# Optimization experiments

Hardware: AMD Instinct MI355X
Metric: run time of the kernel (lower is better)

Reference implementation:

```python
import jax, jax.numpy as jnp
import numpy as np

B, N, M, C, H = 2, 256, 512, 256, 8
Dh = C // H          # head dim = 32
F = 256              # frequency_embedding_size
MAX_PERIOD = 10000.0


def setup_inputs() -> dict:
    rng = jax.random.key(0)
    ks = jax.random.split(rng, 12)
    s = 0.02

    def w(k, shape):
        return jax.random.normal(k, shape, jnp.float32) * s

    inp = {
        "query": jax.random.normal(ks[0], (B, N, C), jnp.float32),
        "key": jax.random.normal(ks[1], (B, M, C), jnp.float32),
        "query_pos": jax.random.uniform(ks[2], (B, N, M), jnp.float32),
        # attention projections (torch Linear stores W as (out,in))
        "Wq": w(ks[3], (C, C)), "bq": jnp.zeros((C,), jnp.float32),
        "Wk": w(ks[4], (C, C)),
        "Wv": w(ks[5], (C, C)), "bv": jnp.zeros((C,), jnp.float32),
        "Wo": w(ks[6], (C, C)), "bo": jnp.zeros((C,), jnp.float32),
        # ScalarEmbedder MLP: Linear(F, C) -> SiLU -> Linear(C, C)
        "W1": w(ks[7], (C, F)), "b1": jnp.zeros((C,), jnp.float32),
        "W2": w(ks[8], (C, C)), "b2": jnp.zeros((C,), jnp.float32),
        "freqs": jnp.exp(-np.log(MAX_PERIOD) * jnp.arange(F // 2, dtype=jnp.float32) / (F // 2)),
    }
    return inp


def reference(query, key, query_pos, Wq, bq, Wk, Wv, bv, Wo, bo, W1, b1, W2, b2, freqs):
    scale = Dh ** (-0.5)
    # projections -> (B, H, N/M, Dh)
    q = (query @ Wq.T + bq).reshape(B, N, H, Dh).transpose(0, 2, 1, 3)
    k = (key @ Wk.T).reshape(B, M, H, Dh).transpose(0, 2, 1, 3)
    v = (key @ Wv.T + bv).reshape(B, M, H, Dh).transpose(0, 2, 1, 3)
    # scalar positional embedding per (n, m) pair
    t = query_pos.reshape(-1)                              # (B*N*M,)
    tf = t[:, None] * freqs                                # (B*N*M, F/2)
    emb = jnp.concatenate([jnp.cos(tf), jnp.sin(tf)], -1)  # (B*N*M, F)
    pe = jax.nn.silu(emb @ W1.T + b1) @ W2.T + b2          # (B*N*M, C)
    pe = pe.reshape(B, N, M, H, Dh).transpose(0, 3, 1, 2, 4)  # (B,H,N,M,Dh)
    # gated scores: (q[:,:,:,None] * pe) . k  ==  einsum over d
    attn = jnp.einsum('bhnd,bhnmd,bhmd->bhnm', q, pe, k) * scale
    attn = jax.nn.softmax(attn, axis=-1)
    x = jnp.einsum('bhnm,bhmd->bhnd', attn, v)             # (B,H,N,Dh)
    x = x.transpose(0, 2, 1, 3).reshape(B, N, C)
    return x @ Wo.T + bo + query
```

## Files before the change

kernel.cpp:

```cpp
#include <hip/hip_runtime.h>

#define Bn 2
#define Nn 256
#define Mn 512
#define Cn 256
#define Hn 8
#define MT 64
#define SCALE_ 0.17677669529663687f
#define INV2PI 0.15915494309189535f

typedef short bf16x8 __attribute__((ext_vector_type(8)));
typedef short bf16x4 __attribute__((ext_vector_type(4)));
typedef float f32x4 __attribute__((ext_vector_type(4)));

static __device__ __forceinline__ float b2f(short s) {
    unsigned u = ((unsigned)(unsigned short)s) << 16;
    return __builtin_bit_cast(float, u);
}
static __device__ __forceinline__ short f2b(float f) {
    unsigned u = __builtin_bit_cast(unsigned, f);
    u += 0x7fffu + ((u >> 16) & 1u);
    return (short)(u >> 16);
}
static __device__ __forceinline__ void async16(const void* g, void* l) {
    __builtin_amdgcn_global_load_lds(
        (const __attribute__((address_space(1))) unsigned int*)g,
        (__attribute__((address_space(3))) unsigned int*)l, 16, 0, 0);
}

__global__ __launch_bounds__(256) void prep(
        const float* __restrict__ query, const float* __restrict__ key,
        const float* __restrict__ Wq, const float* __restrict__ bq,
        const float* __restrict__ Wk, const float* __restrict__ Wv,
        const float* __restrict__ bv, const float* __restrict__ W1,
        const float* __restrict__ W2, short* __restrict__ W1b,
        short* __restrict__ W2b, float* __restrict__ qp,
        short* __restrict__ kpb, short* __restrict__ vpb) {
    __shared__ float arow[32][Cn];
    const int bid = blockIdx.x;
    const int t = threadIdx.x;
    if (bid < 256) {
        const int i = bid * 256 + t;
        W1b[i] = f2b(W1[i]);
        W2b[i] = f2b(W2[i]);
        return;
    }
    if (bid < 512) {
        const int id = bid - 256;
        const int r0 = (id >> 2) * 8, c0 = (id & 3) * 64;
        #pragma unroll
        for (int i = 0; i < 8; ++i) arow[i][t] = query[(size_t)(r0 + i) * Cn + t];
        __syncthreads();
        const int col = c0 + (t & 63);
        const int rs = t >> 6;
        float a0 = 0.f, a1 = 0.f;
        const float* wr = Wq + (size_t)col * Cn;
        for (int k = 0; k < Cn; k += 4) {
            const float4 wv = *(const float4*)(wr + k);
            const int r = rs * 2;
            a0 += arow[r][k] * wv.x + arow[r][k+1] * wv.y
                + arow[r][k+2] * wv.z + arow[r][k+3] * wv.w;
            a1 += arow[r+1][k] * wv.x + arow[r+1][k+1] * wv.y
                + arow[r+1][k+2] * wv.z + arow[r+1][k+3] * wv.w;
        }
        const float bvv = bq[col];
        qp[(size_t)(r0 + rs * 2) * Cn + col] = a0 + bvv;
        qp[(size_t)(r0 + rs * 2 + 1) * Cn + col] = a1 + bvv;
        return;
    }
    const int isv = bid >= 768;
    const int id = bid - (isv ? 768 : 512);
    const int r0 = (id >> 3) * 32, c0 = (id & 7) * 32;
    const float* W = isv ? Wv : Wk;
    short* outb = isv ? vpb : kpb;
    #pragma unroll
    for (int i = 0; i < 32; ++i) arow[i][t] = key[(size_t)(r0 + i) * Cn + t];
    __syncthreads();
    const int col = c0 + (t & 31);
    const int rs = t >> 5;
    float a4[4] = {0.f, 0.f, 0.f, 0.f};
    const float* wr = W + (size_t)col * Cn;
    for (int k = 0; k < Cn; k += 4) {
        const float4 wv = *(const float4*)(wr + k);
        #pragma unroll
        for (int i = 0; i < 4; ++i) {
            const int r = rs * 4 + i;
            a4[i] += arow[r][k] * wv.x + arow[r][k+1] * wv.y
                   + arow[r][k+2] * wv.z + arow[r][k+3] * wv.w;
        }
    }
    const float bvv = isv ? bv[col] : 0.f;
    const int bk = r0 >> 9, m0 = (r0 & 511) + rs * 4;
    char* base = (char*)outb + (size_t)bk * Mn * Cn * 2;
    #pragma unroll
    for (int i = 0; i < 4; ++i) {
        const int m = m0 + i;
        *(short*)(base + m * 512 + ((col * 2) ^ ((m & 7) << 4))) = f2b(a4[i] + bvv);
    }
}

__global__ __launch_bounds__(512)
__attribute__((amdgpu_waves_per_eu(2, 2)))
void fused_attn(
        const float* __restrict__ qp, const short* __restrict__ kpb,
        const short* __restrict__ vpb, const float* __restrict__ qpos,
        const short* __restrict__ W1b, const short* __restrict__ W2b,
        const float* __restrict__ b1, const float* __restrict__ b2,
        const float* __restrict__ freqs, const float* __restrict__ Wo,
        const float* __restrict__ bo, const float* __restrict__ query,
        float* __restrict__ xout) {
    __shared__ __align__(16) char embS[MT * 512];
    __shared__ __align__(16) char kS[MT * 512];
    __shared__ __align__(16) char vS[MT * 512];
    __shared__ float tposS[Mn];
    __shared__ float fbuf[128];
    __shared__ float scb2[Hn * MT];
    __shared__ float pacc[512];
    __shared__ float corrS[Hn], lS[Hn];

    const int t = threadIdx.x;
    const int lane = t & 63;
    const int w = t >> 6;
    const int lr = lane & 15, lg = lane >> 4;

    const int qrow = ((blockIdx.x & 7) << 6) | (blockIdx.x >> 3);
    const int b = qrow >> 8;

    const int cA = w * 32 + lr, cB = cA + 16;
    const short* w1p0 = W1b + (size_t)cA * Cn + lg * 8;
    const short* w1p1 = W1b + (size_t)cB * Cn + lg * 8;
    const short* w2p0 = W2b + (size_t)cA * Cn + lg * 8;
    const short* w2p1 = W2b + (size_t)cB * Cn + lg * 8;

    bf16x8 wreg[16];
    #pragma unroll
    for (int kk = 0; kk < 8; ++kk) {
        wreg[kk] = *(const bf16x8*)(w1p0 + kk * 32);
        wreg[8 + kk] = *(const bf16x8*)(w1p1 + kk * 32);
    }

    const float b1v0 = b1[cA], b1v1 = b1[cB];
    float qr[8], b2r[8];
    #pragma unroll
    for (int i = 0; i < 8; ++i) {
        const int c = w * 32 + (i >> 2) * 16 + lg * 4 + (i & 3);
        qr[i] = qp[(size_t)qrow * Cn + c] * SCALE_;
        b2r[i] = b2[c];
    }
    tposS[t] = qpos[(size_t)qrow * Mn + t];
    if (t < 128) fbuf[t] = freqs[t] * INV2PI;
    float m_run = -1e30f, l_run = 0.f;
    float xacc = 0.f;
    __syncthreads();

    for (int m0 = 0; m0 < Mn; m0 += MT) {
        {
            const size_t tbase = ((size_t)(b * Mn + m0)) * Cn * 2;
            #pragma unroll
            for (int i = 0; i < 4; ++i) {
                const int seg = (i * 8 + w) * 1024;
                async16((const char*)kpb + tbase + seg + lane * 16, kS + seg);
                async16((const char*)vpb + tbase + seg + lane * 16, vS + seg);
            }
        }

        {
            const int m = t >> 3, fg = t & 7;
            const float tv = tposS[m0 + m];
            bf16x8 pc[2], ps[2];
            #pragma unroll
            for (int j = 0; j < 16; ++j) {
                const float xr = tv * fbuf[fg * 16 + j];
                pc[j >> 3][j & 7] = f2b(__builtin_amdgcn_cosf(xr));
                ps[j >> 3][j & 7] = f2b(__builtin_amdgcn_sinf(xr));
            }
            char* rowp = embS + m * 512;
            const int sw = (m & 7) << 4;
            *(bf16x8*)(rowp + ((fg * 32) ^ sw)) = pc[0];
            *(bf16x8*)(rowp + ((fg * 32 + 16) ^ sw)) = pc[1];
            *(bf16x8*)(rowp + ((256 + fg * 32) ^ sw)) = ps[0];
            *(bf16x8*)(rowp + ((256 + fg * 32 + 16) ^ sw)) = ps[1];
        }
        __syncthreads();

        f32x4 acc[4][2];
        #pragma unroll
        for (int pb = 0; pb < 4; ++pb) {
            acc[pb][0] = (f32x4){0.f, 0.f, 0.f, 0.f};
            acc[pb][1] = (f32x4){0.f, 0.f, 0.f, 0.f};
        }
        #pragma unroll
        for (int pb = 0; pb < 4; ++pb) {
            const int row = pb * 16 + lr;
            const int sw = (row & 7) << 4;
            const char* rowp = embS + row * 512;
            #pragma unroll
            for (int kk = 0; kk < 8; ++kk) {
                const bf16x8 a = *(const bf16x8*)(rowp + ((lg * 16 + kk * 64) ^ sw));
                acc[pb][0] = __builtin_amdgcn_mfma_f32_16x16x32_bf16(a, wreg[kk],     acc[pb][0], 0, 0, 0);
                acc[pb][1] = __builtin_amdgcn_mfma_f32_16x16x32_bf16(a, wreg[8 + kk], acc[pb][1], 0, 0, 0);
            }
        }
        #pragma unroll
        for (int kk = 0; kk < 8; ++kk) {
            wreg[kk] = *(const bf16x8*)(w2p0 + kk * 32);
            wreg[8 + kk] = *(const bf16x8*)(w2p1 + kk * 32);
        }
        __syncthreads();

        #pragma unroll
        for (int pb = 0; pb < 4; ++pb) {
            #pragma unroll
            for (int jb = 0; jb < 2; ++jb) {
                const float bv = jb ? b1v1 : b1v0;
                const int j = w * 32 + jb * 16 + lr;
                #pragma unroll
                for (int r = 0; r < 4; ++r) {
                    const int row = pb * 16 + lg * 4 + r;
                    float hv = acc[pb][jb][r] + bv;
                    hv = hv / (1.f + __expf(-hv));
                    *(short*)(embS + row * 512 + ((j * 2) ^ ((row & 7) << 4))) = f2b(hv);
                }
            }
        }
        __syncthreads();

        #pragma unroll
        for (int mb = 0; mb < 4; ++mb)
            #pragma unroll
            for (int cb = 0; cb < 2; ++cb)
                #pragma unroll
                for (int r = 0; r < 4; ++r)
                    acc[mb][cb][r] = b2r[cb * 4 + r];
        #pragma unroll
        for (int mb = 0; mb < 4; ++mb) {
            const int row = mb * 16 + lr;
            const int sw = (row & 7) << 4;
            const char* rowp = embS + row * 512;
            #pragma unroll
            for (int kk = 0; kk < 8; ++kk) {
                const bf16x8 a = *(const bf16x8*)(rowp + ((lg * 16 + kk * 64) ^ sw));
                acc[mb][0] = __builtin_amdgcn_mfma_f32_16x16x32_bf16(wreg[kk],     a, acc[mb][0], 0, 0, 0);
                acc[mb][1] = __builtin_amdgcn_mfma_f32_16x16x32_bf16(wreg[8 + kk], a, acc[mb][1], 0, 0, 0);
            }
        }
        #pragma unroll
        for (int kk = 0; kk < 8; ++kk) {
            wreg[kk] = *(const bf16x8*)(w1p0 + kk * 32);
            wreg[8 + kk] = *(const bf16x8*)(w1p1 + kk * 32);
        }

        #pragma unroll
        for (int mb = 0; mb < 4; ++mb) {
            const int m = mb * 16 + lr;
            const int sw = (m & 7) << 4;
            const char* kr = kS + m * 512;
            const int c0 = (w * 32 + lg * 4) * 2;
            const bf16x4 k0 = *(const bf16x4*)(kr + (c0 ^ sw));
            const bf16x4 k1 = *(const bf16x4*)(kr + ((c0 + 32) ^ sw));
            float partial = 0.f;
            #pragma unroll
            for (int r = 0; r < 4; ++r) {
                partial += qr[r] * b2f(k0[r]) * acc[mb][0][r]
                         + qr[4 + r] * b2f(k1[r]) * acc[mb][1][r];
            }
            partial += __shfl_xor(partial, 16);
            partial += __shfl_xor(partial, 32);
            if (lg == 0) scb2[w * MT + m] = partial;
        }

        {
            const float s = scb2[w * MT + lane];
            float tmax = s;
            #pragma unroll
            for (int msk = 1; msk < 64; msk <<= 1) tmax = fmaxf(tmax, __shfl_xor(tmax, msk));
            const float mnew = fmaxf(m_run, tmax);
            const float corr = __expf(m_run - mnew);
            const float e = __expf(s - mnew);
            scb2[w * MT + lane] = e;
            float ss = e;
            #pragma unroll
            for (int msk = 1; msk < 64; msk <<= 1) ss += __shfl_xor(ss, msk);
            l_run = l_run * corr + ss;
            m_run = mnew;
            if (lane == 0) corrS[w] = corr;
        }
        __syncthreads();

        {
            const int c = t & 255, half = t >> 8;
            const int h = c >> 5;
            const int cx = c * 2;
            const char* vb = vS + (half * 32) * 512;
            const float* wr2 = scb2 + h * MT + half * 32;
            float s = 0.f;
            #pragma unroll
            for (int i = 0; i < 8; ++i) {
                const float4 wa = *(const float4*)(wr2 + i * 4);
                const int mb4 = i * 4;
                s += wa.x * b2f(*(const short*)(vb + (mb4 + 0) * 512 + (cx ^ (((mb4 + 0) & 7) << 4))))
                   + wa.y * b2f(*(const short*)(vb + (mb4 + 1) * 512 + (cx ^ (((mb4 + 1) & 7) << 4))))
                   + wa.z * b2f(*(const short*)(vb + (mb4 + 2) * 512 + (cx ^ (((mb4 + 2) & 7) << 4))))
                   + wa.w * b2f(*(const short*)(vb + (mb4 + 3) * 512 + (cx ^ (((mb4 + 3) & 7) << 4))));
            }
            pacc[t] = s;
        }
        __syncthreads();
        if (t < 256) xacc = xacc * corrS[t >> 5] + pacc[t] + pacc[t + 256];
    }

    if (lane == 0) lS[w] = l_run;
    __syncthreads();
    if (t < 256) scb2[t] = xacc / lS[t >> 5];
    __syncthreads();
    {
        const int j = t & 255, half = t >> 8;
        const float* wr = Wo + (size_t)j * Cn + half * 128;
        const float* xb = scb2 + half * 128;
        float s = 0.f;
        for (int k = 0; k < 128; k += 4) {
            const float4 wv = *(const float4*)(wr + k);
            s += xb[k] * wv.x + xb[k+1] * wv.y + xb[k+2] * wv.z + xb[k+3] * wv.w;
        }
        pacc[t] = s;
    }
    __syncthreads();
    if (t < 256)
        xout[(size_t)qrow * Cn + t] = pacc[t] + pacc[t + 256] + bo[t]
                                    + query[(size_t)qrow * Cn + t];
}

extern "C" void kernel_launch(void* const* d_in, const int* in_sizes, int n_in,
                              void* d_out, int out_size, void* d_ws, size_t ws_size,
                              hipStream_t stream) {
    const float* query = (const float*)d_in[0];
    const float* key   = (const float*)d_in[1];
    const float* qpos  = (const float*)d_in[2];
    const float* Wq    = (const float*)d_in[3];
    const float* bq    = (const float*)d_in[4];
    const float* Wk    = (const float*)d_in[5];
    const float* Wv    = (const float*)d_in[6];
    const float* bv    = (const float*)d_in[7];
    const float* Wo    = (const float*)d_in[8];
    const float* bo    = (const float*)d_in[9];
    const float* W1    = (const float*)d_in[10];
    const float* b1    = (const float*)d_in[11];
    const float* W2    = (const float*)d_in[12];
    const float* b2    = (const float*)d_in[13];
    const float* freqs = (const float*)d_in[14];
    float* out = (float*)d_out;

    char* ws = (char*)d_ws;
    float* qp  = (float*)(ws);
    short* kpb = (short*)(ws + 524288);
    short* vpb = (short*)(ws + 1048576);
    short* W1b = (short*)(ws + 1572864);
    short* W2b = (short*)(ws + 1703936);

    prep<<<1024, 256, 0, stream>>>(query, key, Wq, bq, Wk, Wv, bv, W1, W2,
                                   W1b, W2b, qp, kpb, vpb);
    fused_attn<<<Bn * Nn, 512, 0, stream>>>(qp, kpb, vpb, qpos, W1b, W2b,
                                            b1, b2, freqs, Wo, bo, query, out);
}
```

Before: 325.8 us.

## Double key tile size, fuse Q projection into attention, read V from global

The key tile grows from 64 to 128 rows, which halves the number of loop iterations and barriers per query row. The Q projection moves out of the prep kernel and into the attention kernel, and the weight casts are vectorized. V is now read straight from global memory in an unswizzled layout instead of being staged through LDS. This frees LDS for the larger embedding and K tiles. Weight registers are reloaded every iteration behind an opaque offset to cap register pressure, at the cost of more global and L2 traffic, and each block now does redundant Wq work.

```diff
diff --git a/kernel.cpp b/kernel.cpp
--- a/kernel.cpp
+++ b/kernel.cpp
@@ -5,7 +5,7 @@
 #define Mn 512
 #define Cn 256
 #define Hn 8
-#define MT 64
+#define MT 128
 #define SCALE_ 0.17677669529663687f
 #define INV2PI 0.15915494309189535f
 
@@ -28,51 +28,32 @@
         (__attribute__((address_space(3))) unsigned int*)l, 16, 0, 0);
 }
 
-__global__ __launch_bounds__(256) void prep(
-        const float* __restrict__ query, const float* __restrict__ key,
-        const float* __restrict__ Wq, const float* __restrict__ bq,
-        const float* __restrict__ Wk, const float* __restrict__ Wv,
-        const float* __restrict__ bv, const float* __restrict__ W1,
-        const float* __restrict__ W2, short* __restrict__ W1b,
-        short* __restrict__ W2b, float* __restrict__ qp,
+__global__ __launch_bounds__(256) void prep2(
+        const float* __restrict__ key, const float* __restrict__ Wk,
+        const float* __restrict__ Wv, const float* __restrict__ bv,
+        const float* __restrict__ W1, const float* __restrict__ W2,
+        short* __restrict__ W1b, short* __restrict__ W2b,
         short* __restrict__ kpb, short* __restrict__ vpb) {
     __shared__ float arow[32][Cn];
     const int bid = blockIdx.x;
     const int t = threadIdx.x;
-    if (bid < 256) {
-        const int i = bid * 256 + t;
-        W1b[i] = f2b(W1[i]);
-        W2b[i] = f2b(W2[i]);
+    if (bid < 64) {
+        const int half = bid >> 5;
+        const int off = (bid & 31) * 2048 + t * 8;
+        const float* src = half ? W2 : W1;
+        short* dst = half ? W2b : W1b;
+        const float4 a = *(const float4*)(src + off);
+        const float4 c = *(const float4*)(src + off + 4);
+        bf16x8 p;
+        p[0] = f2b(a.x); p[1] = f2b(a.y); p[2] = f2b(a.z); p[3] = f2b(a.w);
+        p[4] = f2b(c.x); p[5] = f2b(c.y); p[6] = f2b(c.z); p[7] = f2b(c.w);
+        *(bf16x8*)(dst + off) = p;
         return;
     }
-    if (bid < 512) {
-        const int id = bid - 256;
-        const int r0 = (id >> 2) * 8, c0 = (id & 3) * 64;
-        #pragma unroll
-        for (int i = 0; i < 8; ++i) arow[i][t] = query[(size_t)(r0 + i) * Cn + t];
-        __syncthreads();
-        const int col = c0 + (t & 63);
-        const int rs = t >> 6;
-        float a0 = 0.f, a1 = 0.f;
-        const float* wr = Wq + (size_t)col * Cn;
-        for (int k = 0; k < Cn; k += 4) {
-            const float4 wv = *(const float4*)(wr + k);
-            const int r = rs * 2;
-            a0 += arow[r][k] * wv.x + arow[r][k+1] * wv.y
-                + arow[r][k+2] * wv.z + arow[r][k+3] * wv.w;
-            a1 += arow[r+1][k] * wv.x + arow[r+1][k+1] * wv.y
-                + arow[r+1][k+2] * wv.z + arow[r+1][k+3] * wv.w;
-        }
-        const float bvv = bq[col];
-        qp[(size_t)(r0 + rs * 2) * Cn + col] = a0 + bvv;
-        qp[(size_t)(r0 + rs * 2 + 1) * Cn + col] = a1 + bvv;
-        return;
-    }
-    const int isv = bid >= 768;
-    const int id = bid - (isv ? 768 : 512);
+    const int isv = bid >= 320;
+    const int id = bid - (isv ? 320 : 64);
     const int r0 = (id >> 3) * 32, c0 = (id & 7) * 32;
     const float* W = isv ? Wv : Wk;
-    short* outb = isv ? vpb : kpb;
     #pragma unroll
     for (int i = 0; i < 32; ++i) arow[i][t] = key[(size_t)(r0 + i) * Cn + t];
     __syncthreads();
@@ -89,31 +70,36 @@
                    + arow[r][k+2] * wv.z + arow[r][k+3] * wv.w;
         }
     }
-    const float bvv = isv ? bv[col] : 0.f;
-    const int bk = r0 >> 9, m0 = (r0 & 511) + rs * 4;
-    char* base = (char*)outb + (size_t)bk * Mn * Cn * 2;
-    #pragma unroll
-    for (int i = 0; i < 4; ++i) {
-        const int m = m0 + i;
-        *(short*)(base + m * 512 + ((col * 2) ^ ((m & 7) << 4))) = f2b(a4[i] + bvv);
-    }
-}
-
-__global__ __launch_bounds__(512)
-__attribute__((amdgpu_waves_per_eu(2, 2)))
-void fused_attn(
-        const float* __restrict__ qp, const short* __restrict__ kpb,
+    if (!isv) {
+        const int bk = r0 >> 9, mm0 = (r0 & 511) + rs * 4;
+        char* base = (char*)kpb + (size_t)bk * Mn * Cn * 2;
+        #pragma unroll
+        for (int i = 0; i < 4; ++i) {
+            const int m = mm0 + i;
+            *(short*)(base + m * 512 + ((col * 2) ^ ((m & 7) << 4))) = f2b(a4[i]);
+        }
+    } else {
+        const float bvv = bv[col];
+        #pragma unroll
+        for (int i = 0; i < 4; ++i)
+            vpb[(size_t)(r0 + rs * 4 + i) * Cn + col] = f2b(a4[i] + bvv);
+    }
+}
+
+__global__ __launch_bounds__(512, 1) void fused_attn(
+        const float* __restrict__ query, const float* __restrict__ Wq,
+        const float* __restrict__ bq, const short* __restrict__ kpb,
         const short* __restrict__ vpb, const float* __restrict__ qpos,
         const short* __restrict__ W1b, const short* __restrict__ W2b,
         const float* __restrict__ b1, const float* __restrict__ b2,
         const float* __restrict__ freqs, const float* __restrict__ Wo,
-        const float* __restrict__ bo, const float* __restrict__ query,
-        float* __restrict__ xout) {
+        const float* __restrict__ bo, float* __restrict__ xout) {
     __shared__ __align__(16) char embS[MT * 512];
     __shared__ __align__(16) char kS[MT * 512];
-    __shared__ __align__(16) char vS[MT * 512];
     __shared__ float tposS[Mn];
     __shared__ float fbuf[128];
+    __shared__ float qbuf[Cn];
+    __shared__ float b2buf[Cn];
     __shared__ float scb2[Hn * MT];
     __shared__ float pacc[512];
     __shared__ float corrS[Hn], lS[Hn];
@@ -131,66 +117,80 @@
     const short* w1p1 = W1b + (size_t)cB * Cn + lg * 8;
     const short* w2p0 = W2b + (size_t)cA * Cn + lg * 8;
     const short* w2p1 = W2b + (size_t)cB * Cn + lg * 8;
-
-    bf16x8 wreg[16];
-    #pragma unroll
-    for (int kk = 0; kk < 8; ++kk) {
-        wreg[kk] = *(const bf16x8*)(w1p0 + kk * 32);
-        wreg[8 + kk] = *(const bf16x8*)(w1p1 + kk * 32);
-    }
-
     const float b1v0 = b1[cA], b1v1 = b1[cB];
-    float qr[8], b2r[8];
-    #pragma unroll
-    for (int i = 0; i < 8; ++i) {
-        const int c = w * 32 + (i >> 2) * 16 + lg * 4 + (i & 3);
-        qr[i] = qp[(size_t)qrow * Cn + c] * SCALE_;
-        b2r[i] = b2[c];
-    }
+
     tposS[t] = qpos[(size_t)qrow * Mn + t];
     if (t < 128) fbuf[t] = freqs[t] * INV2PI;
+    if (t < 256) {
+        b2buf[t] = b2[t];
+        scb2[t] = query[(size_t)qrow * Cn + t];
+    }
+    __syncthreads();
+    {
+        const int c = t & 255, half = t >> 8;
+        const float* wr = Wq + (size_t)c * Cn + half * 128;
+        const float* xb = scb2 + half * 128;
+        float s = 0.f;
+        for (int k = 0; k < 128; k += 4) {
+            const float4 wv = *(const float4*)(wr + k);
+            s += xb[k] * wv.x + xb[k+1] * wv.y + xb[k+2] * wv.z + xb[k+3] * wv.w;
+        }
+        pacc[t] = s;
+    }
+    __syncthreads();
+    if (t < 256) qbuf[t] = (pacc[t] + pacc[t + 256] + bq[t]) * SCALE_;
+
     float m_run = -1e30f, l_run = 0.f;
     float xacc = 0.f;
-    __syncthreads();
+    bf16x8 wreg[16];
 
     for (int m0 = 0; m0 < Mn; m0 += MT) {
         {
             const size_t tbase = ((size_t)(b * Mn + m0)) * Cn * 2;
             #pragma unroll
-            for (int i = 0; i < 4; ++i) {
+            for (int i = 0; i < 8; ++i) {
                 const int seg = (i * 8 + w) * 1024;
                 async16((const char*)kpb + tbase + seg + lane * 16, kS + seg);
-                async16((const char*)vpb + tbase + seg + lane * 16, vS + seg);
-            }
-        }
-
-        {
-            const int m = t >> 3, fg = t & 7;
+            }
+        }
+
+        {
+            const int m = t >> 2, fq = t & 3;
             const float tv = tposS[m0 + m];
-            bf16x8 pc[2], ps[2];
-            #pragma unroll
-            for (int j = 0; j < 16; ++j) {
-                const float xr = tv * fbuf[fg * 16 + j];
-                pc[j >> 3][j & 7] = f2b(__builtin_amdgcn_cosf(xr));
-                ps[j >> 3][j & 7] = f2b(__builtin_amdgcn_sinf(xr));
-            }
             char* rowp = embS + m * 512;
             const int sw = (m & 7) << 4;
-            *(bf16x8*)(rowp + ((fg * 32) ^ sw)) = pc[0];
-            *(bf16x8*)(rowp + ((fg * 32 + 16) ^ sw)) = pc[1];
-            *(bf16x8*)(rowp + ((256 + fg * 32) ^ sw)) = ps[0];
-            *(bf16x8*)(rowp + ((256 + fg * 32 + 16) ^ sw)) = ps[1];
-        }
-        __syncthreads();
-
-        f32x4 acc[4][2];
-        #pragma unroll
-        for (int pb = 0; pb < 4; ++pb) {
+            #pragma unroll
+            for (int j8 = 0; j8 < 4; ++j8) {
+                bf16x8 pc, ps;
+                #pragma unroll
+                for (int e = 0; e < 8; ++e) {
+                    const float xr = tv * fbuf[fq * 32 + j8 * 8 + e];
+                    pc[e] = f2b(__builtin_amdgcn_cosf(xr));
+                    ps[e] = f2b(__builtin_amdgcn_sinf(xr));
+                }
+                *(bf16x8*)(rowp + ((fq * 64 + j8 * 16) ^ sw)) = pc;
+                *(bf16x8*)(rowp + ((256 + fq * 64 + j8 * 16) ^ sw)) = ps;
+            }
+        }
+        __syncthreads();
+
+        {
+            int woff = 0;
+            asm volatile("" : "+v"(woff));
+            #pragma unroll
+            for (int kk = 0; kk < 8; ++kk) {
+                wreg[kk] = *(const bf16x8*)(w1p0 + woff + kk * 32);
+                wreg[8 + kk] = *(const bf16x8*)(w1p1 + woff + kk * 32);
+            }
+        }
+        f32x4 acc[8][2];
+        #pragma unroll
+        for (int pb = 0; pb < 8; ++pb) {
             acc[pb][0] = (f32x4){0.f, 0.f, 0.f, 0.f};
             acc[pb][1] = (f32x4){0.f, 0.f, 0.f, 0.f};
         }
         #pragma unroll
-        for (int pb = 0; pb < 4; ++pb) {
+        for (int pb = 0; pb < 8; ++pb) {
             const int row = pb * 16 + lr;
             const int sw = (row & 7) << 4;
             const char* rowp = embS + row * 512;
@@ -201,15 +201,10 @@
                 acc[pb][1] = __builtin_amdgcn_mfma_f32_16x16x32_bf16(a, wreg[8 + kk], acc[pb][1], 0, 0, 0);
             }
         }
-        #pragma unroll
-        for (int kk = 0; kk < 8; ++kk) {
-            wreg[kk] = *(const bf16x8*)(w2p0 + kk * 32);
-            wreg[8 + kk] = *(const bf16x8*)(w2p1 + kk * 32);
-        }
-        __syncthreads();
-
-        #pragma unroll
-        for (int pb = 0; pb < 4; ++pb) {
+        __syncthreads();
+
+        #pragma unroll
+        for (int pb = 0; pb < 8; ++pb) {
             #pragma unroll
             for (int jb = 0; jb < 2; ++jb) {
                 const float bv = jb ? b1v1 : b1v0;
@@ -225,15 +220,30 @@
         }
         __syncthreads();
 
-        #pragma unroll
-        for (int mb = 0; mb < 4; ++mb)
-            #pragma unroll
-            for (int cb = 0; cb < 2; ++cb)
+        {
+            int woff = 0;
+            asm volatile("" : "+v"(woff));
+            #pragma unroll
+            for (int kk = 0; kk < 8; ++kk) {
+                wreg[kk] = *(const bf16x8*)(w2p0 + woff + kk * 32);
+                wreg[8 + kk] = *(const bf16x8*)(w2p1 + woff + kk * 32);
+            }
+        }
+        {
+            float b2a[8];
+            #pragma unroll
+            for (int i = 0; i < 8; ++i)
+                b2a[i] = b2buf[w * 32 + (i >> 2) * 16 + lg * 4 + (i & 3)];
+            #pragma unroll
+            for (int mb = 0; mb < 8; ++mb)
                 #pragma unroll
-                for (int r = 0; r < 4; ++r)
-                    acc[mb][cb][r] = b2r[cb * 4 + r];
-        #pragma unroll
-        for (int mb = 0; mb < 4; ++mb) {
+                for (int cb = 0; cb < 2; ++cb)
+                    #pragma unroll
+                    for (int r = 0; r < 4; ++r)
+                        acc[mb][cb][r] = b2a[cb * 4 + r];
+        }
+        #pragma unroll
+        for (int mb = 0; mb < 8; ++mb) {
             const int row = mb * 16 + lr;
             const int sw = (row & 7) << 4;
             const char* rowp = embS + row * 512;
@@ -244,41 +254,45 @@
                 acc[mb][1] = __builtin_amdgcn_mfma_f32_16x16x32_bf16(wreg[8 + kk], a, acc[mb][1], 0, 0, 0);
             }
         }
-        #pragma unroll
-        for (int kk = 0; kk < 8; ++kk) {
-            wreg[kk] = *(const bf16x8*)(w1p0 + kk * 32);
-            wreg[8 + kk] = *(const bf16x8*)(w1p1 + kk * 32);
-        }
-
-        #pragma unroll
-        for (int mb = 0; mb < 4; ++mb) {
-            const int m = mb * 16 + lr;
-            const int sw = (m & 7) << 4;
-            const char* kr = kS + m * 512;
-            const int c0 = (w * 32 + lg * 4) * 2;
-            const bf16x4 k0 = *(const bf16x4*)(kr + (c0 ^ sw));
-            const bf16x4 k1 = *(const bf16x4*)(kr + ((c0 + 32) ^ sw));
-            float partial = 0.f;
-            #pragma unroll
-            for (int r = 0; r < 4; ++r) {
-                partial += qr[r] * b2f(k0[r]) * acc[mb][0][r]
-                         + qr[4 + r] * b2f(k1[r]) * acc[mb][1][r];
-            }
-            partial += __shfl_xor(partial, 16);
-            partial += __shfl_xor(partial, 32);
-            if (lg == 0) scb2[w * MT + m] = partial;
-        }
-
-        {
-            const float s = scb2[w * MT + lane];
-            float tmax = s;
+
+        {
+            float qa[8];
+            #pragma unroll
+            for (int i = 0; i < 8; ++i)
+                qa[i] = qbuf[w * 32 + (i >> 2) * 16 + lg * 4 + (i & 3)];
+            #pragma unroll
+            for (int mb = 0; mb < 8; ++mb) {
+                const int m = mb * 16 + lr;
+                const int sw = (m & 7) << 4;
+                const char* kr = kS + m * 512;
+                const int cc0 = (w * 32 + lg * 4) * 2;
+                const bf16x4 k0 = *(const bf16x4*)(kr + (cc0 ^ sw));
+                const bf16x4 k1 = *(const bf16x4*)(kr + ((cc0 + 32) ^ sw));
+                float partial = 0.f;
+                #pragma unroll
+                for (int r = 0; r < 4; ++r) {
+                    partial += qa[r] * b2f(k0[r]) * acc[mb][0][r]
+                             + qa[4 + r] * b2f(k1[r]) * acc[mb][1][r];
+                }
+                partial += __shfl_xor(partial, 16);
+                partial += __shfl_xor(partial, 32);
+                if (lg == 0) scb2[w * MT + m] = partial;
+            }
+        }
+
+        {
+            const float s0 = scb2[w * MT + lane];
+            const float s1 = scb2[w * MT + 64 + lane];
+            float tmax = fmaxf(s0, s1);
             #pragma unroll
             for (int msk = 1; msk < 64; msk <<= 1) tmax = fmaxf(tmax, __shfl_xor(tmax, msk));
             const float mnew = fmaxf(m_run, tmax);
             const float corr = __expf(m_run - mnew);
-            const float e = __expf(s - mnew);
-            scb2[w * MT + lane] = e;
-            float ss = e;
+            const float e0 = __expf(s0 - mnew);
+            const float e1 = __expf(s1 - mnew);
+            scb2[w * MT + lane] = e0;
+            scb2[w * MT + 64 + lane] = e1;
+            float ss = e0 + e1;
             #pragma unroll
             for (int msk = 1; msk < 64; msk <<= 1) ss += __shfl_xor(ss, msk);
             l_run = l_run * corr + ss;
@@ -290,18 +304,16 @@
         {
             const int c = t & 255, half = t >> 8;
             const int h = c >> 5;
-            const int cx = c * 2;
-            const char* vb = vS + (half * 32) * 512;
-            const float* wr2 = scb2 + h * MT + half * 32;
+            const short* vrow = vpb + ((size_t)(b * Mn + m0 + half * 64)) * Cn + c;
+            const float* wr2 = scb2 + h * MT + half * 64;
             float s = 0.f;
             #pragma unroll
-            for (int i = 0; i < 8; ++i) {
+            for (int i = 0; i < 16; ++i) {
                 const float4 wa = *(const float4*)(wr2 + i * 4);
-                const int mb4 = i * 4;
-                s += wa.x * b2f(*(const short*)(vb + (mb4 + 0) * 512 + (cx ^ (((mb4 + 0) & 7) << 4))))
-                   + wa.y * b2f(*(const short*)(vb + (mb4 + 1) * 512 + (cx ^ (((mb4 + 1) & 7) << 4))))
-                   + wa.z * b2f(*(const short*)(vb + (mb4 + 2) * 512 + (cx ^ (((mb4 + 2) & 7) << 4))))
-                   + wa.w * b2f(*(const short*)(vb + (mb4 + 3) * 512 + (cx ^ (((mb4 + 3) & 7) << 4))));
+                s += wa.x * b2f(vrow[(size_t)(i * 4 + 0) * Cn])
+                   + wa.y * b2f(vrow[(size_t)(i * 4 + 1) * Cn])
+                   + wa.z * b2f(vrow[(size_t)(i * 4 + 2) * Cn])
+                   + wa.w * b2f(vrow[(size_t)(i * 4 + 3) * Cn]);
             }
             pacc[t] = s;
         }
@@ -351,14 +363,12 @@
     float* out = (float*)d_out;
 
     char* ws = (char*)d_ws;
-    float* qp  = (float*)(ws);
-    short* kpb = (short*)(ws + 524288);
-    short* vpb = (short*)(ws + 1048576);
-    short* W1b = (short*)(ws + 1572864);
-    short* W2b = (short*)(ws + 1703936);
-
-    prep<<<1024, 256, 0, stream>>>(query, key, Wq, bq, Wk, Wv, bv, W1, W2,
-                                   W1b, W2b, qp, kpb, vpb);
-    fused_attn<<<Bn * Nn, 512, 0, stream>>>(qp, kpb, vpb, qpos, W1b, W2b,
-                                            b1, b2, freqs, Wo, bo, query, out);
-}
+    short* kpb = (short*)(ws);
+    short* vpb = (short*)(ws + 524288);
+    short* W1b = (short*)(ws + 1048576);
+    short* W2b = (short*)(ws + 1179648);
+
+    prep2<<<576, 256, 0, stream>>>(key, Wk, Wv, bv, W1, W2, W1b, W2b, kpb, vpb);
+    fused_attn<<<Bn * Nn, 512, 0, stream>>>(query, Wq, bq, kpb, vpb, qpos,
+                                            W1b, W2b, b1, b2, freqs, Wo, bo, out);
+}
```

Result: faster. 295.9 us (-9.2%).
